# Optimization experiments

Hardware: AMD Instinct MI355X
Metric: run time of the kernel (lower is better)

The kernel has to match this reference:

```python
import jax, jax.numpy as jnp
import numpy as np


def setup_inputs() -> dict:
    key = jax.random.key(0)
    W0 = jax.random.normal(key, (8192, 8192), dtype=jnp.float32)
    return {"W0": W0}


def reference(W0) -> jnp.ndarray:
    # Faithful to the torch code: elementwise exp (NOT matrix_exp), then trace.
    if W0.ndim == 3 and W0.shape[2] == 1:
        W0 = W0[:, :, 0]
    N = W0.shape[0]
    # trace(exp(W*W)) only touches the diagonal after elementwise exp,
    # but we compute the full elementwise map as the original does; the
    # mathematically equivalent reduced form is sum(exp(diag(W)**2)).
    tr = jnp.trace(jnp.exp(W0 * W0))
    return (tr - N) ** 2.0
```

## Files before the change

kernel.cpp:

```cpp
#include <hip/hip_runtime.h>
#include <math.h>


__global__ __launch_bounds__(64) void diag_partial_kernel(
    const float* __restrict__ W, double* __restrict__ partials, int N) {
    const int lane = threadIdx.x;
    const int i = blockIdx.x * 64 + lane;
    const size_t stride = (size_t)N + 1;

    double acc = 0.0;
    if (i < N) {
        float x = W[(size_t)i * stride];
        acc = (double)expf(x * x);
    }

    #pragma unroll
    for (int off = 32; off > 0; off >>= 1)
        acc += __shfl_down(acc, off, 64);

    if (lane == 0) partials[blockIdx.x] = acc;
}

__global__ __launch_bounds__(64) void diag_final_kernel(
    const double* __restrict__ partials, float* __restrict__ out,
    int nparts, int N) {
    const int lane = threadIdx.x;
    double acc = 0.0;
    for (int p = lane; p < nparts; p += 64)
        acc += partials[p];

    #pragma unroll
    for (int off = 32; off > 0; off >>= 1)
        acc += __shfl_down(acc, off, 64);

    if (lane == 0) {
        double d = acc - (double)N;
        out[0] = (float)(d * d);
    }
}

extern "C" void kernel_launch(void* const* d_in, const int* in_sizes, int n_in,
                              void* d_out, int out_size, void* d_ws, size_t ws_size,
                              hipStream_t stream) {
    const float* W = (const float*)d_in[0];
    float* out = (float*)d_out;
    double* partials = (double*)d_ws;

    long long total = (long long)in_sizes[0];
    int N = (int)(sqrt((double)total) + 0.5);

    int nblocks = (N + 63) / 64;
    diag_partial_kernel<<<nblocks, 64, 0, stream>>>(W, partials, N);
    diag_final_kernel<<<1, 64, 0, stream>>>(partials, out, nblocks, N);
}
```

Before: 11.55 us.

## Fuse diagonal partial and final reduction via last-block atomic counter

Merges the two kernel launches into one. Each block publishes its partial sum with a release store and bumps a global atomic counter, and the block that arrives last reduces all partials and writes the loss. This removes a second launch and its inter-kernel gap from a very short workload. In exchange it adds an atomic per block and relies on the counter's modulo wraparound, since the counter is never reset and must start at zero in the workspace.

```diff
diff --git a/kernel.cpp b/kernel.cpp
--- a/kernel.cpp
+++ b/kernel.cpp
@@ -2,10 +2,13 @@
 #include <math.h>
 
 
-__global__ __launch_bounds__(64) void diag_partial_kernel(
-    const float* __restrict__ W, double* __restrict__ partials, int N) {
+__global__ __launch_bounds__(64) void diag_loss_onepass(
+    const float* __restrict__ W, float* __restrict__ out,
+    unsigned* __restrict__ counter, double* __restrict__ partials, int N) {
     const int lane = threadIdx.x;
-    const int i = blockIdx.x * 64 + lane;
+    const int bid  = blockIdx.x;
+    const int nb   = gridDim.x;
+    const int i    = bid * 64 + lane;
     const size_t stride = (size_t)N + 1;
 
     double acc = 0.0;
@@ -18,24 +21,29 @@
     for (int off = 32; off > 0; off >>= 1)
         acc += __shfl_down(acc, off, 64);
 
-    if (lane == 0) partials[blockIdx.x] = acc;
-}
+    unsigned old = 0;
+    if (lane == 0) {
+        __hip_atomic_store(&partials[bid], acc,
+                           __ATOMIC_RELEASE, __HIP_MEMORY_SCOPE_AGENT);
+        old = __hip_atomic_fetch_add(counter, 1u,
+                                     __ATOMIC_ACQ_REL, __HIP_MEMORY_SCOPE_AGENT);
+    }
+    old = __shfl(old, 0, 64);
+    const bool is_last = (old % (unsigned)nb) == (unsigned)(nb - 1);
 
-__global__ __launch_bounds__(64) void diag_final_kernel(
-    const double* __restrict__ partials, float* __restrict__ out,
-    int nparts, int N) {
-    const int lane = threadIdx.x;
-    double acc = 0.0;
-    for (int p = lane; p < nparts; p += 64)
-        acc += partials[p];
-
-    #pragma unroll
-    for (int off = 32; off > 0; off >>= 1)
-        acc += __shfl_down(acc, off, 64);
-
-    if (lane == 0) {
-        double d = acc - (double)N;
-        out[0] = (float)(d * d);
+    if (is_last) {
+        __threadfence();
+        double s = 0.0;
+        for (int p = lane; p < nb; p += 64)
+            s += __hip_atomic_load(&partials[p],
+                                   __ATOMIC_RELAXED, __HIP_MEMORY_SCOPE_AGENT);
+        #pragma unroll
+        for (int off = 32; off > 0; off >>= 1)
+            s += __shfl_down(s, off, 64);
+        if (lane == 0) {
+            double d = s - (double)N;
+            out[0] = (float)(d * d);
+        }
     }
 }
 
@@ -44,12 +52,13 @@
                               hipStream_t stream) {
     const float* W = (const float*)d_in[0];
     float* out = (float*)d_out;
-    double* partials = (double*)d_ws;
 
     long long total = (long long)in_sizes[0];
     int N = (int)(sqrt((double)total) + 0.5);
 
+    unsigned* counter = (unsigned*)d_ws;
+    double* partials  = (double*)((char*)d_ws + 64);
+
     int nblocks = (N + 63) / 64;
-    diag_partial_kernel<<<nblocks, 64, 0, stream>>>(W, partials, N);
-    diag_final_kernel<<<1, 64, 0, stream>>>(partials, out, nblocks, N);
+    diag_loss_onepass<<<nblocks, 64, 0, stream>>>(W, out, counter, partials, N);
 }
```

Result: faster. 11.12 us (-3.7%).
